# Kernel optimization log

Measured on AMD Instinct MI355X. Metric: run time of the kernel, lower is better.

Reference implementation:

```python
import jax, jax.numpy as jnp
import numpy as np

B, S, D = 4, 2048, 1024

def setup_inputs() -> dict:
    key = jax.random.key(0)
    kv, kk, kq, kw = jax.random.split(key, 4)
    scale = 1.0 / np.sqrt(D)
    v = jax.random.normal(kv, (B, S, D), dtype=jnp.float32)
    k = jax.random.normal(kk, (B, S, D), dtype=jnp.float32)
    q = jax.random.normal(kq, (B, S, D), dtype=jnp.float32)
    wi = jax.random.normal(kw, (D, D), dtype=jnp.float32) * scale
    mask = jnp.tril(jnp.ones((S, S), dtype=bool))[None, :, :]  # causal [1,S,S]
    return {"v": v, "k": k, "q": q, "wi": wi, "mask": mask}

def reference(v, k, q, wi, mask):
    # project q, k, v with the shared weight wi
    q = q @ wi
    k = k @ wi
    v = v @ wi
    # scaled dot-product scores [B,S,S]
    scores = jnp.einsum('bqd,bkd->bqk', q, k) / jnp.sqrt(jnp.asarray(q.shape[-1], q.dtype))
    scores = jnp.where(mask, scores, jnp.asarray(-1e10, scores.dtype))
    attn = jax.nn.softmax(scores, axis=-1)
    # residual: q + attn @ v
    return q + jnp.einsum('bqk,bkd->bqd', attn, v)
```

## Files before the change

### kernel.cpp

```cpp
#include <hip/hip_runtime.h>
#include <hip/hip_bf16.h>

typedef __hip_bfloat16 bf16;
typedef short bf16x8 __attribute__((ext_vector_type(8)));
typedef float f32x4 __attribute__((ext_vector_type(4)));

#define HT 16384

__device__ __forceinline__ void gload16(const void* g, void* l) {
    __builtin_amdgcn_global_load_lds(
        (const __attribute__((address_space(1))) void*)g,
        (__attribute__((address_space(3))) void*)l, 16, 0, 0);
}

__device__ __forceinline__ void stage_half(char* lds, const bf16* src, int ld,
                                           int rowbase, int k0, int slotIdx,
                                           int tid)
{
    char* dst = lds + (size_t)slotIdx * HT + tid * 16;
    const int sub = tid >> 3;
    const int cb  = ((tid & 7) ^ (sub & 7)) << 4;
    #pragma unroll
    for (int p = 0; p < 2; ++p) {
        const int row = p * 64 + sub;
        const char* g = (const char*)(src + (size_t)(rowbase + row) * ld + k0) + cb;
        gload16(g, dst + p * 8192);
    }
}

__device__ __forceinline__ bf16x8 ldsfrag(const char* lds, int slotIdx,
                                          int row, int ks, int cb0)
{
    return *(const bf16x8*)(lds + (size_t)slotIdx * HT
                            + row * 128 + (cb0 ^ (ks << 6)));
}

__launch_bounds__(512, 2)
__global__ void proj_gemm256(const bf16* __restrict__ A, const bf16* __restrict__ B,
                             bf16* __restrict__ C)
{
    extern __shared__ char lds[];
    const int gx = gridDim.x;
    int id = blockIdx.y * gx + blockIdx.x;
    const int chunk = (gridDim.y * gx) >> 3;
    id = (id & 7) * chunk + (id >> 3);
    const int bj = id % gx, bi = id / gx;
    const int brow = bi * 256, bcol = bj * 256;

    const int tid  = threadIdx.x;
    const int lane = tid & 63;
    const int w    = tid >> 6;
    const int wm   = w >> 2, wn = w & 3;
    const int fr   = lane & 15, fq = lane >> 4;
    const int cb0  = ((fr & 7) ^ fq) << 4;
    const int slotA = wm;
    const int slotB = 2 + (wn >> 1);
    const int rB    = (wn & 1) * 64;
    const int NT    = 16;

    f32x4 acc[8][4] = {};
    bf16x8 af[4][2], bv[4][2];

    stage_half(lds, B, 1024, bcol,       0, 2, tid);
    stage_half(lds, A, 1024, brow,       0, 0, tid);
    stage_half(lds, B, 1024, bcol + 128, 0, 3, tid);
    stage_half(lds, A, 1024, brow + 128, 0, 1, tid);
    stage_half(lds, B, 1024, bcol,      64, 6, tid);
    stage_half(lds, A, 1024, brow,      64, 4, tid);
    asm volatile("s_waitcnt vmcnt(4)" ::: "memory");
    __builtin_amdgcn_s_barrier();

#define QUAD(mh, nh)                                                          \
    _Pragma("unroll") for (int m = 0; m < 4; ++m)                             \
    _Pragma("unroll") for (int n = 0; n < 2; ++n)                             \
    _Pragma("unroll") for (int ks = 0; ks < 2; ++ks)                          \
        acc[(mh)*4+m][(nh)*2+n] = __builtin_amdgcn_mfma_f32_16x16x32_bf16(    \
            af[m][ks], bv[(nh)*2+n][ks], acc[(mh)*4+m][(nh)*2+n], 0, 0, 0);

    for (int t = 0; t < NT; ++t) {
        const int buf = t & 1, nbuf = buf ^ 1;
        const int k1 = min(t + 1, NT - 1) << 6;
        const int k2 = min(t + 2, NT - 1) << 6;

        #pragma unroll
        for (int m = 0; m < 4; ++m)
            #pragma unroll
            for (int ks = 0; ks < 2; ++ks)
                af[m][ks] = ldsfrag(lds, buf * 4 + slotA, m * 16 + fr, ks, cb0);
        #pragma unroll
        for (int n = 0; n < 2; ++n)
            #pragma unroll
            for (int ks = 0; ks < 2; ++ks)
                bv[n][ks] = ldsfrag(lds, buf * 4 + slotB, rB + n * 16 + fr, ks, cb0);
        stage_half(lds, B, 1024, bcol + 128, k1, nbuf * 4 + 3, tid);
        __builtin_amdgcn_s_barrier();
        __builtin_amdgcn_s_setprio(1);
        QUAD(0, 0)
        __builtin_amdgcn_s_setprio(0);
        __builtin_amdgcn_s_barrier();

        #pragma unroll
        for (int n = 2; n < 4; ++n)
            #pragma unroll
            for (int ks = 0; ks < 2; ++ks)
                bv[n][ks] = ldsfrag(lds, buf * 4 + slotB, rB + n * 16 + fr, ks, cb0);
        stage_half(lds, A, 1024, brow + 128, k1, nbuf * 4 + 1, tid);
        __builtin_amdgcn_s_barrier();
        __builtin_amdgcn_s_setprio(1);
        QUAD(0, 1)
        __builtin_amdgcn_s_setprio(0);
        __builtin_amdgcn_s_barrier();

        #pragma unroll
        for (int m = 0; m < 4; ++m)
            #pragma unroll
            for (int ks = 0; ks < 2; ++ks)
                af[m][ks] = ldsfrag(lds, buf * 4 + slotA, (m + 4) * 16 + fr, ks, cb0);
        stage_half(lds, B, 1024, bcol, k2, buf * 4 + 2, tid);
        __builtin_amdgcn_s_barrier();
        __builtin_amdgcn_s_setprio(1);
        QUAD(1, 0)
        __builtin_amdgcn_s_setprio(0);
        __builtin_amdgcn_s_barrier();

        stage_half(lds, A, 1024, brow, k2, buf * 4 + 0, tid);
        __builtin_amdgcn_s_barrier();
        __builtin_amdgcn_s_setprio(1);
        QUAD(1, 1)
        __builtin_amdgcn_s_setprio(0);
        asm volatile("s_waitcnt vmcnt(4)" ::: "memory");
        __builtin_amdgcn_s_barrier();
    }
#undef QUAD

    #pragma unroll
    for (int mf = 0; mf < 8; ++mf) {
        const int r0 = brow + wm * 128 + mf * 16 + fq * 4;
        #pragma unroll
        for (int nf = 0; nf < 4; ++nf) {
            const int c = bcol + wn * 64 + nf * 16 + fr;
            #pragma unroll
            for (int j = 0; j < 4; ++j)
                C[(size_t)(r0 + j) * 1024 + c] = __float2bfloat16(acc[mf][nf][j]);
        }
    }
}

template<int MODE>
__launch_bounds__(512, 2)
__global__ void gemm_bn128(const bf16* __restrict__ A, const bf16* __restrict__ B,
                           bf16* __restrict__ Cb, float* __restrict__ Cf,
                           const bf16* __restrict__ Res,
                           int lda, int ldb, int ldc, int K,
                           long sA, long sB, long sC, long sR, float scale)
{
    extern __shared__ char lds[];
    int bi, bj;
    if (MODE == 1) { bj = blockIdx.x; bi = blockIdx.y; if (bj > 2 * bi + 1) return; }
    else           { bi = blockIdx.x; bj = blockIdx.y; }
    const int bz = blockIdx.z;
    A += (size_t)bz * sA;
    B += (size_t)bz * sB;
    const int brow = bi * 256, bcol = bj * 128;

    const int tid  = threadIdx.x;
    const int lane = tid & 63;
    const int w    = tid >> 6;
    const int wm   = w >> 1, wn = w & 1;
    const int fr   = lane & 15, fq = lane >> 4;
    const int cb0  = ((fr & 7) ^ fq) << 4;
    const int slotA = wm >> 1;
    const int rA    = (wm & 1) * 64;
    const int rB    = wn * 64;

    const int kmax = (MODE == 2) ? (brow + 256) : K;
    const int NT   = kmax >> 6;

    f32x4 acc[4][4] = {};
    bf16x8 af[4][2], bv[4][2];

    stage_half(lds, B, ldb, bcol,       0, 2, tid);
    stage_half(lds, A, lda, brow,       0, 0, tid);
    stage_half(lds, A, lda, brow + 128, 0, 1, tid);
    stage_half(lds, B, ldb, bcol,      64, 5, tid);
    asm volatile("s_waitcnt vmcnt(2)" ::: "memory");
    __builtin_amdgcn_s_barrier();

#define QUAD2(m0, n0)                                                         \
    _Pragma("unroll") for (int dm = 0; dm < 2; ++dm)                          \
    _Pragma("unroll") for (int dn = 0; dn < 2; ++dn)                          \
    _Pragma("unroll") for (int ks = 0; ks < 2; ++ks)                          \
        acc[(m0)+dm][(n0)+dn] = __builtin_amdgcn_mfma_f32_16x16x32_bf16(      \
            af[(m0)+dm][ks], bv[(n0)+dn][ks], acc[(m0)+dm][(n0)+dn], 0, 0, 0);

    for (int t = 0; t < NT; ++t) {
        const int buf = t & 1, nbuf = buf ^ 1;
        const int k1 = min(t + 1, NT - 1) << 6;
        const int k2 = min(t + 2, NT - 1) << 6;

        #pragma unroll
        for (int m = 0; m < 2; ++m)
            #pragma unroll
            for (int ks = 0; ks < 2; ++ks)
                af[m][ks] = ldsfrag(lds, buf * 3 + slotA, rA + m * 16 + fr, ks, cb0);
        #pragma unroll
        for (int n = 0; n < 2; ++n)
            #pragma unroll
            for (int ks = 0; ks < 2; ++ks)
                bv[n][ks] = ldsfrag(lds, buf * 3 + 2, rB + n * 16 + fr, ks, cb0);
        stage_half(lds, A, lda, brow, k1, nbuf * 3 + 0, tid);
        __builtin_amdgcn_s_barrier();
        __builtin_amdgcn_s_setprio(1);
        QUAD2(0, 0)
        __builtin_amdgcn_s_setprio(0);
        __builtin_amdgcn_s_barrier();

        #pragma unroll
        for (int n = 2; n < 4; ++n)
            #pragma unroll
            for (int ks = 0; ks < 2; ++ks)
                bv[n][ks] = ldsfrag(lds, buf * 3 + 2, rB + n * 16 + fr, ks, cb0);
        stage_half(lds, A, lda, brow + 128, k1, nbuf * 3 + 1, tid);
        __builtin_amdgcn_s_barrier();
        __builtin_amdgcn_s_setprio(1);
        QUAD2(0, 2)
        __builtin_amdgcn_s_setprio(0);
        __builtin_amdgcn_s_barrier();

        #pragma unroll
        for (int m = 2; m < 4; ++m)
            #pragma unroll
            for (int ks = 0; ks < 2; ++ks)
                af[m][ks] = ldsfrag(lds, buf * 3 + slotA, rA + m * 16 + fr, ks, cb0);
        stage_half(lds, B, ldb, bcol, k2, buf * 3 + 2, tid);
        __builtin_amdgcn_s_barrier();
        __builtin_amdgcn_s_setprio(1);
        QUAD2(2, 2)
        __builtin_amdgcn_s_setprio(0);
        __builtin_amdgcn_s_barrier();

        __builtin_amdgcn_s_setprio(1);
        QUAD2(2, 0)
        __builtin_amdgcn_s_setprio(0);
        asm volatile("s_waitcnt vmcnt(2)" ::: "memory");
        __builtin_amdgcn_s_barrier();
    }
#undef QUAD2

    if (MODE == 1) {
        bf16* C = Cb + (size_t)bz * sC;
        #pragma unroll
        for (int mf = 0; mf < 4; ++mf) {
            const int r0 = brow + wm * 64 + mf * 16 + fq * 4;
            #pragma unroll
            for (int nf = 0; nf < 4; ++nf) {
                const int c = bcol + wn * 64 + nf * 16 + fr;
                #pragma unroll
                for (int j = 0; j < 4; ++j)
                    C[(size_t)(r0 + j) * ldc + c] =
                        __float2bfloat16(acc[mf][nf][j] * scale);
            }
        }
    } else {
        float* C = Cf + (size_t)bz * sC;
        const bf16* R = Res + (size_t)bz * sR;
        #pragma unroll
        for (int mf = 0; mf < 4; ++mf) {
            const int r0 = brow + wm * 64 + mf * 16 + fq * 4;
            #pragma unroll
            for (int nf = 0; nf < 4; ++nf) {
                const int c = bcol + wn * 64 + nf * 16 + fr;
                #pragma unroll
                for (int j = 0; j < 4; ++j)
                    C[(size_t)(r0 + j) * ldc + c] = acc[mf][nf][j] +
                        __bfloat162float(R[(size_t)(r0 + j) * ldc + c]);
            }
        }
    }
}

__global__ void convert_qkv(const float* __restrict__ q, const float* __restrict__ k,
                            const float* __restrict__ v, bf16* __restrict__ Xb)
{
    const int N8 = 8192 * 1024 / 8;
    const int total = 3 * N8;
    for (int i = blockIdx.x * 256 + threadIdx.x; i < total; i += gridDim.x * 256) {
        const int t = i / N8, j = i - t * N8;
        const float4* s = (t == 0) ? (const float4*)q
                        : (t == 1) ? (const float4*)k : (const float4*)v;
        float4 a = s[2 * j], bq = s[2 * j + 1];
        float vals[8] = {a.x, a.y, a.z, a.w, bq.x, bq.y, bq.z, bq.w};
        union { short h[8]; bf16x8 v8; } o;
        #pragma unroll
        for (int e = 0; e < 8; ++e) {
            bf16 hh = __float2bfloat16(vals[e]);
            o.h[e] = *(short*)&hh;
        }
        ((bf16x8*)Xb)[i] = o.v8;
    }
}

__global__ void transpose_wi(const float* __restrict__ wi, bf16* __restrict__ Wt)
{
    __shared__ float t[32][33];
    const int n0 = blockIdx.x * 32, k0 = blockIdx.y * 32;
    const int lx = threadIdx.x & 31, ly = threadIdx.x >> 5;
    for (int i = ly; i < 32; i += 8)
        t[i][lx] = wi[(size_t)(k0 + i) * 1024 + n0 + lx];
    __syncthreads();
    for (int i = ly; i < 32; i += 8)
        Wt[(size_t)(n0 + i) * 1024 + k0 + lx] = __float2bfloat16(t[lx][i]);
}

__global__ void transpose_vp(const bf16* __restrict__ vp, bf16* __restrict__ vpT)
{
    __shared__ bf16 t[32][33];
    const int b = blockIdx.z;
    const int d0 = blockIdx.x * 32, s0 = blockIdx.y * 32;
    const bf16* src = vp + (size_t)b * 2048 * 1024;
    bf16* dst = vpT + (size_t)b * 1024 * 2048;
    const int lx = threadIdx.x & 31, ly = threadIdx.x >> 5;
    for (int i = ly; i < 32; i += 8)
        t[i][lx] = src[(size_t)(s0 + i) * 1024 + d0 + lx];
    __syncthreads();
    for (int i = ly; i < 32; i += 8)
        dst[(size_t)(d0 + i) * 2048 + s0 + lx] = t[lx][i];
}

__device__ __forceinline__ float bf2f(short s) {
    union { float f; unsigned u; } c;
    c.u = ((unsigned)(unsigned short)s) << 16;
    return c.f;
}

__launch_bounds__(256)
__global__ void softmax_rows(bf16* __restrict__ P)
{
    const int wid = threadIdx.x >> 6, lane = threadIdx.x & 63;
    const int r = blockIdx.x * 4 + wid, b = blockIdx.y;
    bf16* row = P + ((size_t)b * 2048 + r) * 2048;
    const int nv  = r + 1;
    const int rup = (r & ~255) + 256;

    float vals[4][8];
    float m = -1e30f;
    #pragma unroll
    for (int c = 0; c < 4; ++c) {
        const int k0 = c * 512 + lane * 8;
        bf16x8 x = *(const bf16x8*)(row + k0);
        #pragma unroll
        for (int j = 0; j < 8; ++j) {
            float f = (k0 + j < nv) ? bf2f(x[j]) : -1e30f;
            vals[c][j] = f;
            m = fmaxf(m, f);
        }
    }
    #pragma unroll
    for (int o = 32; o; o >>= 1) m = fmaxf(m, __shfl_xor(m, o));

    float sum = 0.f;
    #pragma unroll
    for (int c = 0; c < 4; ++c)
        #pragma unroll
        for (int j = 0; j < 8; ++j) {
            float e = __expf(vals[c][j] - m);
            vals[c][j] = e;
            sum += e;
        }
    #pragma unroll
    for (int o = 32; o; o >>= 1) sum += __shfl_xor(sum, o);
    const float inv = 1.0f / sum;

    #pragma unroll
    for (int c = 0; c < 4; ++c) {
        const int k0 = c * 512 + lane * 8;
        if (k0 < rup) {
            union { short h[8]; bf16x8 v8; } o;
            #pragma unroll
            for (int j = 0; j < 8; ++j) {
                bf16 hh = __float2bfloat16(vals[c][j] * inv);
                o.h[j] = *(short*)&hh;
            }
            *(bf16x8*)(row + k0) = o.v8;
        }
    }
}

extern "C" void kernel_launch(void* const* d_in, const int* in_sizes, int n_in,
                              void* d_out, int out_size, void* d_ws, size_t ws_size,
                              hipStream_t stream)
{
    const float* v  = (const float*)d_in[0];
    const float* k  = (const float*)d_in[1];
    const float* q  = (const float*)d_in[2];
    const float* wi = (const float*)d_in[3];
    float* out = (float*)d_out;

    char* ws = (char*)d_ws;
    const size_t WT_OFF   = 0;
    const size_t PROJ_OFF = WT_OFF + (2u << 20);
    const size_t VPT_OFF  = PROJ_OFF + (size_t)24576 * 1024 * 2;
    const size_t XB_OFF   = VPT_OFF + (size_t)4 * 1024 * 2048 * 2;

    bf16* Wt   = (bf16*)(ws + WT_OFF);
    bf16* proj = (bf16*)(ws + PROJ_OFF);
    bf16* vpT  = (bf16*)(ws + VPT_OFF);
    bf16* Xb   = (bf16*)(ws + XB_OFF);
    bf16* P    = Xb;

    bf16* qp_b = proj;
    bf16* kp_b = proj + (size_t)8192 * 1024;
    bf16* vp_b = proj + (size_t)16384 * 1024;

    (void)hipFuncSetAttribute((const void*)proj_gemm256,
            hipFuncAttributeMaxDynamicSharedMemorySize, 131072);
    (void)hipFuncSetAttribute((const void*)gemm_bn128<1>,
            hipFuncAttributeMaxDynamicSharedMemorySize, 98304);
    (void)hipFuncSetAttribute((const void*)gemm_bn128<2>,
            hipFuncAttributeMaxDynamicSharedMemorySize, 98304);

    transpose_wi<<<dim3(32, 32), 256, 0, stream>>>(wi, Wt);
    convert_qkv<<<2048, 256, 0, stream>>>(q, k, v, Xb);

    proj_gemm256<<<dim3(4, 96), 512, 131072, stream>>>(Xb, Wt, proj);

    transpose_vp<<<dim3(32, 64, 4), 256, 0, stream>>>(vp_b, vpT);

    gemm_bn128<1><<<dim3(16, 8, 4), 512, 98304, stream>>>(
        qp_b, kp_b, P, nullptr, nullptr,
        1024, 1024, 2048, 1024,
        (long)2048 * 1024, (long)2048 * 1024, (long)2048 * 2048, 0, 0.03125f);

    softmax_rows<<<dim3(512, 4), 256, 0, stream>>>(P);

    gemm_bn128<2><<<dim3(8, 8, 4), 512, 98304, stream>>>(
        P, vpT, nullptr, out, qp_b,
        2048, 2048, 1024, 2048,
        (long)2048 * 2048, (long)1024 * 2048, (long)2048 * 1024, (long)2048 * 1024, 1.0f);
}
```

Baseline: 191.9 us.

## Retile projection and attention GEMMs to 128x128 with triangular scheduling

Replaces the 256x256 projection GEMM with a 256x128-tile variant using an XCD-aware block remap. The scores GEMM now launches only lower-triangular 128x128 tiles through a triangular index decode, and the PV GEMM pairs tile rows pid and 15-pid so causal work per block is balanced. Softmax skips loading columns beyond the causal 256-aligned bound. Smaller tiles aim for higher occupancy and less wasted causal work, at the cost of more LDS traffic per flop.

Result: faster. 183.7 us (-4.3%).

```diff
diff --git a/kernel.cpp b/kernel.cpp
--- a/kernel.cpp
+++ b/kernel.cpp
@@ -35,132 +35,20 @@
                             + row * 128 + (cb0 ^ (ks << 6)));
 }
 
+__device__ __forceinline__ float bf2f(short s) {
+    union { float f; unsigned u; } c;
+    c.u = ((unsigned)(unsigned short)s) << 16;
+    return c.f;
+}
+
 __launch_bounds__(512, 2)
-__global__ void proj_gemm256(const bf16* __restrict__ A, const bf16* __restrict__ B,
-                             bf16* __restrict__ C)
+__global__ void proj_bn128(const bf16* __restrict__ A, const bf16* __restrict__ B,
+                           bf16* __restrict__ C)
 {
     extern __shared__ char lds[];
-    const int gx = gridDim.x;
-    int id = blockIdx.y * gx + blockIdx.x;
-    const int chunk = (gridDim.y * gx) >> 3;
-    id = (id & 7) * chunk + (id >> 3);
-    const int bj = id % gx, bi = id / gx;
-    const int brow = bi * 256, bcol = bj * 256;
-
-    const int tid  = threadIdx.x;
-    const int lane = tid & 63;
-    const int w    = tid >> 6;
-    const int wm   = w >> 2, wn = w & 3;
-    const int fr   = lane & 15, fq = lane >> 4;
-    const int cb0  = ((fr & 7) ^ fq) << 4;
-    const int slotA = wm;
-    const int slotB = 2 + (wn >> 1);
-    const int rB    = (wn & 1) * 64;
-    const int NT    = 16;
-
-    f32x4 acc[8][4] = {};
-    bf16x8 af[4][2], bv[4][2];
-
-    stage_half(lds, B, 1024, bcol,       0, 2, tid);
-    stage_half(lds, A, 1024, brow,       0, 0, tid);
-    stage_half(lds, B, 1024, bcol + 128, 0, 3, tid);
-    stage_half(lds, A, 1024, brow + 128, 0, 1, tid);
-    stage_half(lds, B, 1024, bcol,      64, 6, tid);
-    stage_half(lds, A, 1024, brow,      64, 4, tid);
-    asm volatile("s_waitcnt vmcnt(4)" ::: "memory");
-    __builtin_amdgcn_s_barrier();
-
-#define QUAD(mh, nh)                                                          \
-    _Pragma("unroll") for (int m = 0; m < 4; ++m)                             \
-    _Pragma("unroll") for (int n = 0; n < 2; ++n)                             \
-    _Pragma("unroll") for (int ks = 0; ks < 2; ++ks)                          \
-        acc[(mh)*4+m][(nh)*2+n] = __builtin_amdgcn_mfma_f32_16x16x32_bf16(    \
-            af[m][ks], bv[(nh)*2+n][ks], acc[(mh)*4+m][(nh)*2+n], 0, 0, 0);
-
-    for (int t = 0; t < NT; ++t) {
-        const int buf = t & 1, nbuf = buf ^ 1;
-        const int k1 = min(t + 1, NT - 1) << 6;
-        const int k2 = min(t + 2, NT - 1) << 6;
-
-        #pragma unroll
-        for (int m = 0; m < 4; ++m)
-            #pragma unroll
-            for (int ks = 0; ks < 2; ++ks)
-                af[m][ks] = ldsfrag(lds, buf * 4 + slotA, m * 16 + fr, ks, cb0);
-        #pragma unroll
-        for (int n = 0; n < 2; ++n)
-            #pragma unroll
-            for (int ks = 0; ks < 2; ++ks)
-                bv[n][ks] = ldsfrag(lds, buf * 4 + slotB, rB + n * 16 + fr, ks, cb0);
-        stage_half(lds, B, 1024, bcol + 128, k1, nbuf * 4 + 3, tid);
-        __builtin_amdgcn_s_barrier();
-        __builtin_amdgcn_s_setprio(1);
-        QUAD(0, 0)
-        __builtin_amdgcn_s_setprio(0);
-        __builtin_amdgcn_s_barrier();
-
-        #pragma unroll
-        for (int n = 2; n < 4; ++n)
-            #pragma unroll
-            for (int ks = 0; ks < 2; ++ks)
-                bv[n][ks] = ldsfrag(lds, buf * 4 + slotB, rB + n * 16 + fr, ks, cb0);
-        stage_half(lds, A, 1024, brow + 128, k1, nbuf * 4 + 1, tid);
-        __builtin_amdgcn_s_barrier();
-        __builtin_amdgcn_s_setprio(1);
-        QUAD(0, 1)
-        __builtin_amdgcn_s_setprio(0);
-        __builtin_amdgcn_s_barrier();
-
-        #pragma unroll
-        for (int m = 0; m < 4; ++m)
-            #pragma unroll
-            for (int ks = 0; ks < 2; ++ks)
-                af[m][ks] = ldsfrag(lds, buf * 4 + slotA, (m + 4) * 16 + fr, ks, cb0);
-        stage_half(lds, B, 1024, bcol, k2, buf * 4 + 2, tid);
-        __builtin_amdgcn_s_barrier();
-        __builtin_amdgcn_s_setprio(1);
-        QUAD(1, 0)
-        __builtin_amdgcn_s_setprio(0);
-        __builtin_amdgcn_s_barrier();
-
-        stage_half(lds, A, 1024, brow, k2, buf * 4 + 0, tid);
-        __builtin_amdgcn_s_barrier();
-        __builtin_amdgcn_s_setprio(1);
-        QUAD(1, 1)
-        __builtin_amdgcn_s_setprio(0);
-        asm volatile("s_waitcnt vmcnt(4)" ::: "memory");
-        __builtin_amdgcn_s_barrier();
-    }
-#undef QUAD
-
-    #pragma unroll
-    for (int mf = 0; mf < 8; ++mf) {
-        const int r0 = brow + wm * 128 + mf * 16 + fq * 4;
-        #pragma unroll
-        for (int nf = 0; nf < 4; ++nf) {
-            const int c = bcol + wn * 64 + nf * 16 + fr;
-            #pragma unroll
-            for (int j = 0; j < 4; ++j)
-                C[(size_t)(r0 + j) * 1024 + c] = __float2bfloat16(acc[mf][nf][j]);
-        }
-    }
-}
-
-template<int MODE>
-__launch_bounds__(512, 2)
-__global__ void gemm_bn128(const bf16* __restrict__ A, const bf16* __restrict__ B,
-                           bf16* __restrict__ Cb, float* __restrict__ Cf,
-                           const bf16* __restrict__ Res,
-                           int lda, int ldb, int ldc, int K,
-                           long sA, long sB, long sC, long sR, float scale)
-{
-    extern __shared__ char lds[];
-    int bi, bj;
-    if (MODE == 1) { bj = blockIdx.x; bi = blockIdx.y; if (bj > 2 * bi + 1) return; }
-    else           { bi = blockIdx.x; bj = blockIdx.y; }
-    const int bz = blockIdx.z;
-    A += (size_t)bz * sA;
-    B += (size_t)bz * sB;
+    const int orig = blockIdx.y * 8 + blockIdx.x;
+    const int wk = (orig & 7) * 96 + (orig >> 3);
+    const int bi = wk >> 3, bj = wk & 7;
     const int brow = bi * 256, bcol = bj * 128;
 
     const int tid  = threadIdx.x;
@@ -172,17 +60,15 @@
     const int slotA = wm >> 1;
     const int rA    = (wm & 1) * 64;
     const int rB    = wn * 64;
-
-    const int kmax = (MODE == 2) ? (brow + 256) : K;
-    const int NT   = kmax >> 6;
+    const int NT    = 16;
 
     f32x4 acc[4][4] = {};
     bf16x8 af[4][2], bv[4][2];
 
-    stage_half(lds, B, ldb, bcol,       0, 2, tid);
-    stage_half(lds, A, lda, brow,       0, 0, tid);
-    stage_half(lds, A, lda, brow + 128, 0, 1, tid);
-    stage_half(lds, B, ldb, bcol,      64, 5, tid);
+    stage_half(lds, B, 1024, bcol,       0, 2, tid);
+    stage_half(lds, A, 1024, brow,       0, 0, tid);
+    stage_half(lds, A, 1024, brow + 128, 0, 1, tid);
+    stage_half(lds, B, 1024, bcol,      64, 5, tid);
     asm volatile("s_waitcnt vmcnt(2)" ::: "memory");
     __builtin_amdgcn_s_barrier();
 
@@ -208,7 +94,7 @@
             #pragma unroll
             for (int ks = 0; ks < 2; ++ks)
                 bv[n][ks] = ldsfrag(lds, buf * 3 + 2, rB + n * 16 + fr, ks, cb0);
-        stage_half(lds, A, lda, brow, k1, nbuf * 3 + 0, tid);
+        stage_half(lds, A, 1024, brow, k1, nbuf * 3 + 0, tid);
         __builtin_amdgcn_s_barrier();
         __builtin_amdgcn_s_setprio(1);
         QUAD2(0, 0)
@@ -220,7 +106,7 @@
             #pragma unroll
             for (int ks = 0; ks < 2; ++ks)
                 bv[n][ks] = ldsfrag(lds, buf * 3 + 2, rB + n * 16 + fr, ks, cb0);
-        stage_half(lds, A, lda, brow + 128, k1, nbuf * 3 + 1, tid);
+        stage_half(lds, A, 1024, brow + 128, k1, nbuf * 3 + 1, tid);
         __builtin_amdgcn_s_barrier();
         __builtin_amdgcn_s_setprio(1);
         QUAD2(0, 2)
@@ -232,7 +118,7 @@
             #pragma unroll
             for (int ks = 0; ks < 2; ++ks)
                 af[m][ks] = ldsfrag(lds, buf * 3 + slotA, rA + m * 16 + fr, ks, cb0);
-        stage_half(lds, B, ldb, bcol, k2, buf * 3 + 2, tid);
+        stage_half(lds, B, 1024, bcol, k2, buf * 3 + 2, tid);
         __builtin_amdgcn_s_barrier();
         __builtin_amdgcn_s_setprio(1);
         QUAD2(2, 2)
@@ -247,36 +133,161 @@
     }
 #undef QUAD2
 
-    if (MODE == 1) {
-        bf16* C = Cb + (size_t)bz * sC;
-        #pragma unroll
-        for (int mf = 0; mf < 4; ++mf) {
-            const int r0 = brow + wm * 64 + mf * 16 + fq * 4;
-            #pragma unroll
-            for (int nf = 0; nf < 4; ++nf) {
-                const int c = bcol + wn * 64 + nf * 16 + fr;
+    #pragma unroll
+    for (int mf = 0; mf < 4; ++mf) {
+        const int r0 = brow + wm * 64 + mf * 16 + fq * 4;
+        #pragma unroll
+        for (int nf = 0; nf < 4; ++nf) {
+            const int c = bcol + wn * 64 + nf * 16 + fr;
+            #pragma unroll
+            for (int j = 0; j < 4; ++j)
+                C[(size_t)(r0 + j) * 1024 + c] = __float2bfloat16(acc[mf][nf][j]);
+        }
+    }
+}
+
+template<int MODE>
+__device__ __forceinline__ void tile128(char* lds, const bf16* A, const bf16* B,
+                                        bf16* Cb, float* Cf, const bf16* Res,
+                                        int lda, int ldb, int ldcb,
+                                        int brow, int bcol, int NT, float scale,
+                                        int tid, int wm, int wn, int fr, int fq,
+                                        int cb0)
+{
+    f32x4 acc[4][2] = {};
+    bf16x8 af[4][2], bv[2][2];
+
+    stage_half(lds, A, lda, brow, 0,  0, tid);
+    stage_half(lds, B, ldb, bcol, 0,  3, tid);
+    stage_half(lds, A, lda, brow, 64, 1, tid);
+    stage_half(lds, B, ldb, bcol, 64, 4, tid);
+    asm volatile("s_waitcnt vmcnt(4)" ::: "memory");
+    __builtin_amdgcn_s_barrier();
+
+    for (int t = 0; t < NT; ++t) {
+        const int aslot = t % 3, bslot = 3 + (t & 1);
+        const int k2 = min(t + 2, NT - 1) << 6;
+
+        #pragma unroll
+        for (int m = 0; m < 2; ++m)
+            #pragma unroll
+            for (int ks = 0; ks < 2; ++ks)
+                af[m][ks] = ldsfrag(lds, aslot, wm * 64 + m * 16 + fr, ks, cb0);
+        #pragma unroll
+        for (int n = 0; n < 2; ++n)
+            #pragma unroll
+            for (int ks = 0; ks < 2; ++ks)
+                bv[n][ks] = ldsfrag(lds, bslot, wn * 32 + n * 16 + fr, ks, cb0);
+        stage_half(lds, A, lda, brow, k2, (t + 2) % 3, tid);
+        __builtin_amdgcn_s_barrier();
+        __builtin_amdgcn_s_setprio(1);
+        #pragma unroll
+        for (int m = 0; m < 2; ++m)
+            #pragma unroll
+            for (int n = 0; n < 2; ++n)
                 #pragma unroll
-                for (int j = 0; j < 4; ++j)
-                    C[(size_t)(r0 + j) * ldc + c] =
+                for (int ks = 0; ks < 2; ++ks)
+                    acc[m][n] = __builtin_amdgcn_mfma_f32_16x16x32_bf16(
+                        af[m][ks], bv[n][ks], acc[m][n], 0, 0, 0);
+        __builtin_amdgcn_s_setprio(0);
+        __builtin_amdgcn_s_barrier();
+
+        #pragma unroll
+        for (int m = 2; m < 4; ++m)
+            #pragma unroll
+            for (int ks = 0; ks < 2; ++ks)
+                af[m][ks] = ldsfrag(lds, aslot, wm * 64 + m * 16 + fr, ks, cb0);
+        stage_half(lds, B, ldb, bcol, k2, bslot, tid);
+        __builtin_amdgcn_s_barrier();
+        __builtin_amdgcn_s_setprio(1);
+        #pragma unroll
+        for (int m = 2; m < 4; ++m)
+            #pragma unroll
+            for (int n = 0; n < 2; ++n)
+                #pragma unroll
+                for (int ks = 0; ks < 2; ++ks)
+                    acc[m][n] = __builtin_amdgcn_mfma_f32_16x16x32_bf16(
+                        af[m][ks], bv[n][ks], acc[m][n], 0, 0, 0);
+        __builtin_amdgcn_s_setprio(0);
+        asm volatile("s_waitcnt vmcnt(4)" ::: "memory");
+        __builtin_amdgcn_s_barrier();
+    }
+
+    #pragma unroll
+    for (int mf = 0; mf < 4; ++mf) {
+        const int r0 = brow + wm * 64 + mf * 16 + fq * 4;
+        #pragma unroll
+        for (int nf = 0; nf < 2; ++nf) {
+            const int c = bcol + wn * 32 + nf * 16 + fr;
+            #pragma unroll
+            for (int j = 0; j < 4; ++j) {
+                if (MODE == 1)
+                    Cb[(size_t)(r0 + j) * ldcb + c] =
                         __float2bfloat16(acc[mf][nf][j] * scale);
+                else
+                    Cf[(size_t)(r0 + j) * ldcb + c] = acc[mf][nf][j] +
+                        __bfloat162float(Res[(size_t)(r0 + j) * ldcb + c]);
             }
         }
-    } else {
-        float* C = Cf + (size_t)bz * sC;
-        const bf16* R = Res + (size_t)bz * sR;
-        #pragma unroll
-        for (int mf = 0; mf < 4; ++mf) {
-            const int r0 = brow + wm * 64 + mf * 16 + fq * 4;
-            #pragma unroll
-            for (int nf = 0; nf < 4; ++nf) {
-                const int c = bcol + wn * 64 + nf * 16 + fr;
-                #pragma unroll
-                for (int j = 0; j < 4; ++j)
-                    C[(size_t)(r0 + j) * ldc + c] = acc[mf][nf][j] +
-                        __bfloat162float(R[(size_t)(r0 + j) * ldc + c]);
-            }
-        }
-    }
+    }
+}
+
+__launch_bounds__(512, 4)
+__global__ void scores128(const bf16* __restrict__ qp, const bf16* __restrict__ kp,
+                          bf16* __restrict__ P)
+{
+    extern __shared__ char lds[];
+    const int j = blockIdx.x;
+    int bi = (int)((__fsqrt_rn(8.0f * j + 1.0f) - 1.0f) * 0.5f);
+    while ((bi + 1) * (bi + 2) / 2 <= j) ++bi;
+    while (bi * (bi + 1) / 2 > j) --bi;
+    const int bj = j - bi * (bi + 1) / 2;
+    const int bz = blockIdx.z;
+
+    const int tid  = threadIdx.x;
+    const int lane = tid & 63;
+    const int w    = tid >> 6;
+    const int wm   = w >> 2, wn = w & 3;
+    const int fr   = lane & 15, fq = lane >> 4;
+    const int cb0  = ((fr & 7) ^ fq) << 4;
+
+    tile128<1>(lds,
+               qp + (size_t)bz * 2048 * 1024,
+               kp + (size_t)bz * 2048 * 1024,
+               P + (size_t)bz * 2048 * 2048, nullptr, nullptr,
+               1024, 1024, 2048,
+               bi * 128, bj * 128, 16, 0.03125f,
+               tid, wm, wn, fr, fq, cb0);
+}
+
+__launch_bounds__(512, 4)
+__global__ void pv128(const bf16* __restrict__ P, const bf16* __restrict__ V,
+                      const bf16* __restrict__ R, float* __restrict__ C)
+{
+    extern __shared__ char lds[];
+    const int pid = blockIdx.x, bj = blockIdx.y, bz = blockIdx.z;
+    const bf16* Pb = P + (size_t)bz * 2048 * 2048;
+    const bf16* Vb = V + (size_t)bz * 1024 * 2048;
+    const bf16* Rb = R + (size_t)bz * 2048 * 1024;
+    float* Cb = C + (size_t)bz * 2048 * 1024;
+
+    const int tid  = threadIdx.x;
+    const int lane = tid & 63;
+    const int w    = tid >> 6;
+    const int wm   = w >> 2, wn = w & 3;
+    const int fr   = lane & 15, fq = lane >> 4;
+    const int cb0  = ((fr & 7) ^ fq) << 4;
+    const int bcol = bj * 128;
+
+    tile128<2>(lds, Pb, Vb, nullptr, Cb, Rb, 2048, 2048, 1024,
+               pid * 128, bcol, 2 * (pid + 1), 1.0f,
+               tid, wm, wn, fr, fq, cb0);
+    asm volatile("s_waitcnt vmcnt(0) lgkmcnt(0)" ::: "memory");
+    __builtin_amdgcn_s_barrier();
+    const int bi2 = 15 - pid;
+    tile128<2>(lds, Pb, Vb, nullptr, Cb, Rb, 2048, 2048, 1024,
+               bi2 * 128, bcol, 2 * (bi2 + 1), 1.0f,
+               tid, wm, wn, fr, fq, cb0);
 }
 
 __global__ void convert_qkv(const float* __restrict__ q, const float* __restrict__ k,
@@ -327,12 +338,6 @@
         dst[(size_t)(d0 + i) * 2048 + s0 + lx] = t[lx][i];
 }
 
-__device__ __forceinline__ float bf2f(short s) {
-    union { float f; unsigned u; } c;
-    c.u = ((unsigned)(unsigned short)s) << 16;
-    return c.f;
-}
-
 __launch_bounds__(256)
 __global__ void softmax_rows(bf16* __restrict__ P)
 {
@@ -347,12 +352,17 @@
     #pragma unroll
     for (int c = 0; c < 4; ++c) {
         const int k0 = c * 512 + lane * 8;
-        bf16x8 x = *(const bf16x8*)(row + k0);
-        #pragma unroll
-        for (int j = 0; j < 8; ++j) {
-            float f = (k0 + j < nv) ? bf2f(x[j]) : -1e30f;
-            vals[c][j] = f;
-            m = fmaxf(m, f);
+        if (k0 < rup) {
+            bf16x8 x = *(const bf16x8*)(row + k0);
+            #pragma unroll
+            for (int j = 0; j < 8; ++j) {
+                float f = (k0 + j < nv) ? bf2f(x[j]) : -1e30f;
+                vals[c][j] = f;
+                m = fmaxf(m, f);
+            }
+        } else {
+            #pragma unroll
+            for (int j = 0; j < 8; ++j) vals[c][j] = -1e30f;
         }
     }
     #pragma unroll
@@ -412,29 +422,23 @@
     bf16* kp_b = proj + (size_t)8192 * 1024;
     bf16* vp_b = proj + (size_t)16384 * 1024;
 
-    (void)hipFuncSetAttribute((const void*)proj_gemm256,
-            hipFuncAttributeMaxDynamicSharedMemorySize, 131072);
-    (void)hipFuncSetAttribute((const void*)gemm_bn128<1>,
+    (void)hipFuncSetAttribute((const void*)proj_bn128,
             hipFuncAttributeMaxDynamicSharedMemorySize, 98304);
-    (void)hipFuncSetAttribute((const void*)gemm_bn128<2>,
-            hipFuncAttributeMaxDynamicSharedMemorySize, 98304);
+    (void)hipFuncSetAttribute((const void*)scores128,
+            hipFuncAttributeMaxDynamicSharedMemorySize, 81920);
+    (void)hipFuncSetAttribute((const void*)pv128,
+            hipFuncAttributeMaxDynamicSharedMemorySize, 81920);
 
     transpose_wi<<<dim3(32, 32), 256, 0, stream>>>(wi, Wt);
     convert_qkv<<<2048, 256, 0, stream>>>(q, k, v, Xb);
 
-    proj_gemm256<<<dim3(4, 96), 512, 131072, stream>>>(Xb, Wt, proj);
+    proj_bn128<<<dim3(8, 96), 512, 98304, stream>>>(Xb, Wt, proj);
 
     transpose_vp<<<dim3(32, 64, 4), 256, 0, stream>>>(vp_b, vpT);
 
-    gemm_bn128<1><<<dim3(16, 8, 4), 512, 98304, stream>>>(
-        qp_b, kp_b, P, nullptr, nullptr,
-        1024, 1024, 2048, 1024,
-        (long)2048 * 1024, (long)2048 * 1024, (long)2048 * 2048, 0, 0.03125f);
+    scores128<<<dim3(136, 1, 4), 512, 81920, stream>>>(qp_b, kp_b, P);
 
     softmax_rows<<<dim3(512, 4), 256, 0, stream>>>(P);
 
-    gemm_bn128<2><<<dim3(8, 8, 4), 512, 98304, stream>>>(
-        P, vpT, nullptr, out, qp_b,
-        2048, 2048, 1024, 2048,
-        (long)2048 * 2048, (long)1024 * 2048, (long)2048 * 1024, (long)2048 * 1024, 1.0f);
-}
+    pv128<<<dim3(8, 8, 4), 512, 81920, stream>>>(P, vpT, qp_b, out);
+}
```
